# Optimization experiments

Hardware: AMD Instinct MI355X
Metric: run time of the kernel (lower is better)

The kernel has to match this reference:

```python
import math
import jax, jax.numpy as jnp
import numpy as np

TOPK = 2
CAPACITY_FACTOR = 1.25
MIN_CAPACITY = 4


def setup_inputs() -> dict:
    key = jax.random.key(0)
    k1, k2, k3, k4, k5 = jax.random.split(key, 5)
    B, T, H, W, D = 2, 8, 16, 16, 2048
    E, I = 16, 2048
    s = 1.0 / math.sqrt(D)
    return {
        "hidden_states": jax.random.normal(k1, (B, T, H, W, D), dtype=jnp.float32),
        "wg_weight": jax.random.normal(k2, (E, D), dtype=jnp.float32) * s,
        "gate_proj": jax.random.normal(k3, (E, I, D), dtype=jnp.float32) * s,
        "up_proj": jax.random.normal(k4, (E, I, D), dtype=jnp.float32) * s,
        "down_proj": jax.random.normal(k5, (E, D, I), dtype=jnp.float32) * (1.0 / math.sqrt(I)),
    }


def _moe_forward(x, wg, gp, up, dp):
    B, T, H, W, D = x.shape
    S = T * H * W
    # core_shape=(1,1,1): indexing tokens == calculate tokens, flatten (T,H,W)
    tokens = x.reshape(B, S, D).transpose(1, 0, 2).reshape(-1, D)  # (N, D)
    N = tokens.shape[0]
    E = wg.shape[0]

    logits = tokens.astype(jnp.float32) @ wg.T              # (N, E)
    gates = jax.nn.softmax(logits, axis=1)                  # (N, E)

    # static expert capacity: topk * max(ceil(N/E * cf), min_capacity)
    cap = TOPK * max(math.ceil(N / E * CAPACITY_FACTOR), MIN_CAPACITY)

    _, expert_index = jax.lax.top_k(gates, TOPK)            # (N, k)
    expert_mask = jax.nn.one_hot(expert_index, E, dtype=jnp.int32)  # (N, k, E)

    # aux load-balance loss (computed for fidelity)
    mask_aux = expert_mask.max(axis=1).astype(jnp.float32)  # (N, E)
    l_aux = (E ** 2) * jnp.mean(jnp.mean(mask_aux, axis=0) * jnp.mean(gates, axis=0))

    # normalize top-k probabilities (norm_topk_prob=True, topk>1)
    gates_s = jnp.clip(jnp.einsum('nke,ne->n', expert_mask.astype(gates.dtype), gates),
                       jnp.finfo(gates.dtype).eps)
    router_probs = gates / gates_s[:, None]                 # (N, E)

    # token priority: cumsum over (topk*N) flattened in topk-major order
    em = expert_mask.transpose(1, 0, 2).reshape(TOPK * N, E)  # (kN, E)
    tp = jnp.cumsum(em, axis=0) * em - 1
    tp = tp.reshape(TOPK, N, E).transpose(1, 0, 2).max(axis=1)  # (N, E)
    valid = (tp >= 0) & (tp < cap)
    tp = jnp.where(valid, tp, 0)
    dispatch_mask = (tp[:, :, None] == jnp.arange(cap)[None, None, :]) & valid[:, :, None]  # (N,E,C) bool
    combine_weights = router_probs[:, :, None] * dispatch_mask  # (N, E, C)

    # dispatch -> expert FFN (SwiGLU) -> combine
    dm = dispatch_mask.astype(tokens.dtype)
    dispatched = jnp.einsum('nec,nd->ecd', dm, tokens)      # (E, C, D)
    gate_out = jax.nn.silu(jnp.einsum('ecd,eid->eci', dispatched, gp))
    up_out = jnp.einsum('ecd,eid->eci', dispatched, up)
    expert_out = jnp.einsum('eci,edi->ecd', gate_out * up_out, dp)  # (E, C, D)
    combined = jnp.einsum('nec,ecd->nd', combine_weights, expert_out)  # (N, D)

    y = combined.reshape(S, B, D).transpose(1, 0, 2).reshape(B, T, H, W, D)
    return y, l_aux


def reference(hidden_states, wg_weight, gate_proj, up_proj, down_proj):
    y, _l_aux = _moe_forward(hidden_states, wg_weight, gate_proj, up_proj, down_proj)
    return y
```

## Files before the change

### kernel.cpp

```cpp
#include <hip/hip_runtime.h>
#include <hip/hip_bf16.h>
#include <cstdint>
#include <cstddef>

#define NTOK 4096
#define NEXP 16
#define DIM  2048
#define IDIM 2048
#define CAP  640
#define SEQ  2048

typedef float v4f __attribute__((ext_vector_type(4)));
typedef short v8s __attribute__((ext_vector_type(8)));

__device__ __forceinline__ unsigned short f2b(float x) {
    union { float f; unsigned u; } c; c.f = x;
    unsigned r = c.u + 0x7FFFu + ((c.u >> 16) & 1u);
    return (unsigned short)(r >> 16);
}
__device__ __forceinline__ float b2f(unsigned short x) {
    union { unsigned u; float f; } c; c.u = ((unsigned)x) << 16;
    return c.f;
}

__device__ __forceinline__ void async16(const void* g, void* l) {
    __builtin_amdgcn_global_load_lds(
        (const __attribute__((address_space(1))) unsigned int*)g,
        (__attribute__((address_space(3))) unsigned int*)l,
        16, 0, 0);
}

__global__ __launch_bounds__(256) void router_kernel(
    const float* __restrict__ hidden, const float* __restrict__ wg,
    int* __restrict__ top1, int* __restrict__ top2,
    float* __restrict__ w1, float* __restrict__ w2)
{
    int wid  = threadIdx.x >> 6;
    int lane = threadIdx.x & 63;
    int n = blockIdx.x * 4 + wid;
    int e = lane & 15;
    int chunk = lane >> 4;
    const float* tok  = hidden + ((size_t)(n & 1) * SEQ + (n >> 1)) * DIM;
    const float* wrow = wg + (size_t)e * DIM;
    float acc = 0.f;
    int d0 = chunk * (DIM / 4);
    #pragma unroll 4
    for (int d = d0; d < d0 + DIM / 4; d += 4) {
        float4 t4 = *(const float4*)(tok + d);
        float4 g4 = *(const float4*)(wrow + d);
        acc += t4.x * g4.x + t4.y * g4.y + t4.z * g4.z + t4.w * g4.w;
    }
    acc += __shfl_down(acc, 32);
    acc += __shfl_down(acc, 16);
    float v = acc;
    float v1 = v; int i1 = e;
    #pragma unroll
    for (int off = 8; off; off >>= 1) {
        float ov = __shfl_xor(v1, off);
        int   oi = __shfl_xor(i1, off);
        if (ov > v1 || (ov == v1 && oi < i1)) { v1 = ov; i1 = oi; }
    }
    float v2 = (e == i1) ? -INFINITY : v; int i2 = e;
    #pragma unroll
    for (int off = 8; off; off >>= 1) {
        float ov = __shfl_xor(v2, off);
        int   oi = __shfl_xor(i2, off);
        if (ov > v2 || (ov == v2 && oi < i2)) { v2 = ov; i2 = oi; }
    }
    if (lane == 0) {
        float e2v = expf(v2 - v1);
        float inv = 1.f / (1.f + e2v);
        top1[n] = i1; top2[n] = i2;
        w1[n] = inv;  w2[n] = e2v * inv;
    }
}

__global__ __launch_bounds__(1024) void slot_kernel(
    const int* __restrict__ top1, const int* __restrict__ top2,
    int* __restrict__ slot1, int* __restrict__ slot2,
    int* __restrict__ exp_tok, int* __restrict__ counts)
{
    int w = threadIdx.x >> 6;
    int lane = threadIdx.x & 63;
    unsigned long long below = (lane == 0) ? 0ull : ((~0ull) >> (64 - lane));
    int base = 0;
    for (int c = 0; c < NTOK / 64; ++c) {
        int n = c * 64 + lane;
        bool p = (top1[n] == w);
        unsigned long long m = __ballot(p);
        if (p) {
            int s = base + __popcll(m & below);
            slot1[n] = s;
            if (s < CAP) exp_tok[w * CAP + s] = n;
        }
        base += __popcll(m);
    }
    for (int c = 0; c < NTOK / 64; ++c) {
        int n = c * 64 + lane;
        bool p = (top2[n] == w);
        unsigned long long m = __ballot(p);
        if (p) {
            int s = base + __popcll(m & below);
            slot2[n] = s;
            if (s < CAP) exp_tok[w * CAP + s] = n;
        }
        base += __popcll(m);
    }
    if (lane == 0) counts[w] = base < CAP ? base : CAP;
}

__global__ __launch_bounds__(256) void dispatch_kernel(
    const float* __restrict__ hidden, const int* __restrict__ exp_tok,
    const int* __restrict__ counts, unsigned short* __restrict__ disp)
{
    int s = blockIdx.x, e = blockIdx.y;
    unsigned short* dst = disp + ((size_t)e * CAP + s) * DIM + threadIdx.x * 8;
    if (s < counts[e]) {
        int n = exp_tok[e * CAP + s];
        const float* src = hidden + ((size_t)(n & 1) * SEQ + (n >> 1)) * DIM + threadIdx.x * 8;
        float4 a = *(const float4*)src;
        float4 b = *(const float4*)(src + 4);
        v8s o;
        o[0] = (short)f2b(a.x); o[1] = (short)f2b(a.y);
        o[2] = (short)f2b(a.z); o[3] = (short)f2b(a.w);
        o[4] = (short)f2b(b.x); o[5] = (short)f2b(b.y);
        o[6] = (short)f2b(b.z); o[7] = (short)f2b(b.w);
        *(v8s*)dst = o;
    } else {
        v8s z = {0, 0, 0, 0, 0, 0, 0, 0};
        *(v8s*)dst = z;
    }
}

#define BK 64

template<int NW, int ROUNDS>
__device__ __forceinline__ void stage_a(
    const unsigned short* __restrict__ gbase, int grow0, int k0, int rs,
    unsigned short* lds, int wv, int ln)
{
    int sr = ln >> 3;
    int cb = ln & 7;
    #pragma unroll
    for (int p = 0; p < ROUNDS; ++p) {
        int r = p * (NW * 8) + wv * 8 + sr;
        const unsigned short* g = gbase + (size_t)(grow0 + r) * rs + k0 + ((cb ^ (r & 7)) << 3);
        async16(g, lds + (p * (NW * 8) + wv * 8) * 64);
    }
}

template<int NT, int ROUNDS>
__device__ __forceinline__ void issue_bx(
    const float* __restrict__ gbase, int grow0, int k0, int rs,
    float4* regs, int tid)
{
    int cb = tid & 7;
    int r0 = tid >> 3;
    #pragma unroll
    for (int p = 0; p < ROUNDS; ++p) {
        const float* g = gbase + (size_t)(grow0 + p * (NT / 8) + r0) * rs + k0 + (cb << 3);
        regs[2 * p]     = *(const float4*)g;
        regs[2 * p + 1] = *(const float4*)(g + 4);
    }
}

template<int NT, int ROUNDS>
__device__ __forceinline__ void write_bx(
    const float4* regs, unsigned short* lds, int tid)
{
    int cb = tid & 7;
    int r0 = tid >> 3;
    #pragma unroll
    for (int p = 0; p < ROUNDS; ++p) {
        int r = p * (NT / 8) + r0;
        float4 x = regs[2 * p], y = regs[2 * p + 1];
        v8s o;
        o[0] = (short)f2b(x.x); o[1] = (short)f2b(x.y);
        o[2] = (short)f2b(x.z); o[3] = (short)f2b(x.w);
        o[4] = (short)f2b(y.x); o[5] = (short)f2b(y.y);
        o[6] = (short)f2b(y.z); o[7] = (short)f2b(y.w);
        *(v8s*)&lds[r * 64 + ((cb ^ (r & 7)) << 3)] = o;
    }
}

__device__ __forceinline__ void grid_decomp3(int bid, int& mi, int& ni, int& e) {
    int swz = (bid & 7) * 96 + (bid >> 3);
    mi = swz % 3;
    int t = swz / 3;
    ni = t & 15;
    e  = t >> 4;
}

__global__ __launch_bounds__(512, 2) void gateup_kernel(
    const unsigned short* __restrict__ disp, const float* __restrict__ gp,
    const float* __restrict__ up, const int* __restrict__ counts,
    unsigned short* __restrict__ hbuf)
{
    extern __shared__ unsigned short smem[];
    unsigned short* As0 = smem;
    unsigned short* As1 = smem + 16384;
    unsigned short* Bgs = smem + 32768;
    unsigned short* Bus = smem + 40960;
    int mi, ni, e;
    grid_decomp3(blockIdx.x, mi, ni, e);
    int m0 = mi * 256;
    if (m0 >= counts[e]) return;
    int n0 = ni * 128;
    int tid = threadIdx.x;
    int wv = tid >> 6, ln = tid & 63;
    int wm = wv >> 1, wn = wv & 1;
    int lrow = ln & 15, quad = ln >> 4;
    int sw = lrow & 7;

    const unsigned short* Ab = disp + (size_t)e * CAP * DIM;
    const float* Gb = gp + (size_t)e * IDIM * DIM;
    const float* Ub = up + (size_t)e * IDIM * DIM;

    int arow[4], brow[4];
    #pragma unroll
    for (int i = 0; i < 4; ++i) {
        arow[i] = (wm * 64 + i * 16 + lrow) * 64;
        brow[i] = (wn * 64 + i * 16 + lrow) * 64;
    }

    v4f accg[4][4], accu[4][4];
    #pragma unroll
    for (int i = 0; i < 4; ++i)
        #pragma unroll
        for (int j = 0; j < 4; ++j) { accg[i][j] = (v4f)0.f; accu[i][j] = (v4f)0.f; }

    float4 rg[4], ru[4];
    stage_a<8, 4>(Ab, m0, 0, DIM, As0, wv, ln);
    issue_bx<512, 2>(Gb, n0, 0, DIM, rg, tid);
    issue_bx<512, 2>(Ub, n0, 0, DIM, ru, tid);

    for (int k0 = 0; k0 < DIM; k0 += BK) {
        int cur = (k0 >> 6) & 1;
        unsigned short* Ac = cur ? As1 : As0;
        unsigned short* An = cur ? As0 : As1;
        __syncthreads();
        write_bx<512, 2>(rg, Bgs, tid);
        write_bx<512, 2>(ru, Bus, tid);
        __syncthreads();
        int kn = k0 + BK;
        if (kn < DIM) {
            stage_a<8, 4>(Ab, m0, kn, DIM, An, wv, ln);
            issue_bx<512, 2>(Gb, n0, kn, DIM, rg, tid);
            issue_bx<512, 2>(Ub, n0, kn, DIM, ru, tid);
        }
        #pragma unroll
        for (int ks = 0; ks < BK; ks += 32) {
            int cq = ks >> 3;
            v8s a[4];
            #pragma unroll
            for (int i = 0; i < 4; ++i)
                a[i] = *(const v8s*)&Ac[arow[i] + (((cq + quad) ^ sw) << 3)];
            #pragma unroll
            for (int j = 0; j < 4; ++j) {
                v8s bg = *(const v8s*)&Bgs[brow[j] + (((cq + quad) ^ sw) << 3)];
                v8s bu = *(const v8s*)&Bus[brow[j] + (((cq + quad) ^ sw) << 3)];
                #pragma unroll
                for (int i = 0; i < 4; ++i) {
                    accg[i][j] = __builtin_amdgcn_mfma_f32_16x16x32_bf16(a[i], bg, accg[i][j], 0, 0, 0);
                    accu[i][j] = __builtin_amdgcn_mfma_f32_16x16x32_bf16(a[i], bu, accu[i][j], 0, 0, 0);
                }
            }
        }
    }
    unsigned short* hb = hbuf + (size_t)e * CAP * IDIM;
    #pragma unroll
    for (int i = 0; i < 4; ++i)
        #pragma unroll
        for (int j = 0; j < 4; ++j) {
            int row = m0 + wm * 64 + i * 16 + quad * 4;
            int col = n0 + wn * 64 + j * 16 + lrow;
            #pragma unroll
            for (int rg_ = 0; rg_ < 4; ++rg_) {
                if (row + rg_ < CAP) {
                    float g = accg[i][j][rg_], u = accu[i][j][rg_];
                    float hv = (g / (1.f + __expf(-g))) * u;
                    hb[(size_t)(row + rg_) * IDIM + col] = f2b(hv);
                }
            }
        }
}

__global__ __launch_bounds__(256, 2) void down_kernel(
    const unsigned short* __restrict__ hbuf, const float* __restrict__ dp,
    const int* __restrict__ counts, unsigned short* __restrict__ eo)
{
    extern __shared__ unsigned short smem[];
    unsigned short* As0 = smem;
    unsigned short* As1 = smem + 16384;
    unsigned short* Bs  = smem + 32768;
    int mi, ni, e;
    grid_decomp3(blockIdx.x, mi, ni, e);
    int m0 = mi * 256;
    if (m0 >= counts[e]) return;
    int n0 = ni * 128;
    int tid = threadIdx.x;
    int wv = tid >> 6, ln = tid & 63;
    int wm = wv >> 1, wn = wv & 1;
    int lrow = ln & 15, quad = ln >> 4;
    int sw = lrow & 7;

    const unsigned short* Ab = hbuf + (size_t)e * CAP * IDIM;
    const float* Db = dp + (size_t)e * DIM * IDIM;

    int arow[8], brow[4];
    #pragma unroll
    for (int i = 0; i < 8; ++i)
        arow[i] = (wm * 128 + i * 16 + lrow) * 64;
    #pragma unroll
    for (int j = 0; j < 4; ++j)
        brow[j] = (wn * 64 + j * 16 + lrow) * 64;

    v4f acc[8][4];
    #pragma unroll
    for (int i = 0; i < 8; ++i)
        #pragma unroll
        for (int j = 0; j < 4; ++j) acc[i][j] = (v4f)0.f;

    float4 rb[8];
    stage_a<4, 8>(Ab, m0, 0, IDIM, As0, wv, ln);
    issue_bx<256, 4>(Db, n0, 0, IDIM, rb, tid);

    for (int k0 = 0; k0 < IDIM; k0 += BK) {
        int cur = (k0 >> 6) & 1;
        unsigned short* Ac = cur ? As1 : As0;
        unsigned short* An = cur ? As0 : As1;
        __syncthreads();
        write_bx<256, 4>(rb, Bs, tid);
        __syncthreads();
        int kn = k0 + BK;
        if (kn < IDIM) {
            stage_a<4, 8>(Ab, m0, kn, IDIM, An, wv, ln);
            issue_bx<256, 4>(Db, n0, kn, IDIM, rb, tid);
        }
        #pragma unroll
        for (int ks = 0; ks < BK; ks += 32) {
            int cq = ks >> 3;
            v8s a[8];
            #pragma unroll
            for (int i = 0; i < 8; ++i)
                a[i] = *(const v8s*)&Ac[arow[i] + (((cq + quad) ^ sw) << 3)];
            #pragma unroll
            for (int j = 0; j < 4; ++j) {
                v8s b = *(const v8s*)&Bs[brow[j] + (((cq + quad) ^ sw) << 3)];
                #pragma unroll
                for (int i = 0; i < 8; ++i)
                    acc[i][j] = __builtin_amdgcn_mfma_f32_16x16x32_bf16(a[i], b, acc[i][j], 0, 0, 0);
            }
        }
    }
    unsigned short* ob = eo + (size_t)e * CAP * DIM;
    #pragma unroll
    for (int i = 0; i < 8; ++i)
        #pragma unroll
        for (int j = 0; j < 4; ++j) {
            int row = m0 + wm * 128 + i * 16 + quad * 4;
            int col = n0 + wn * 64 + j * 16 + lrow;
            #pragma unroll
            for (int rg_ = 0; rg_ < 4; ++rg_) {
                if (row + rg_ < CAP)
                    ob[(size_t)(row + rg_) * DIM + col] = f2b(acc[i][j][rg_]);
            }
        }
}

__global__ __launch_bounds__(256) void combine_kernel(
    const unsigned short* __restrict__ eo,
    const int* __restrict__ top1, const int* __restrict__ top2,
    const int* __restrict__ slot1, const int* __restrict__ slot2,
    const float* __restrict__ w1, const float* __restrict__ w2,
    float* __restrict__ out)
{
    int n = blockIdx.x;
    int d = threadIdx.x * 8;
    float acc[8];
    #pragma unroll
    for (int i = 0; i < 8; ++i) acc[i] = 0.f;
    int s1 = slot1[n], s2 = slot2[n];
    if (s1 < CAP) {
        const unsigned short* p = eo + ((size_t)top1[n] * CAP + s1) * DIM + d;
        float w = w1[n];
        v8s v = *(const v8s*)p;
        #pragma unroll
        for (int i = 0; i < 8; ++i) acc[i] += w * b2f((unsigned short)v[i]);
    }
    if (s2 < CAP) {
        const unsigned short* p = eo + ((size_t)top2[n] * CAP + s2) * DIM + d;
        float w = w2[n];
        v8s v = *(const v8s*)p;
        #pragma unroll
        for (int i = 0; i < 8; ++i) acc[i] += w * b2f((unsigned short)v[i]);
    }
    float* o = out + ((size_t)(n & 1) * SEQ + (n >> 1)) * DIM + d;
    float4 o0 = {acc[0], acc[1], acc[2], acc[3]};
    float4 o1 = {acc[4], acc[5], acc[6], acc[7]};
    *(float4*)o = o0;
    *(float4*)(o + 4) = o1;
}

extern "C" void kernel_launch(void* const* d_in, const int* in_sizes, int n_in,
                              void* d_out, int out_size, void* d_ws, size_t ws_size,
                              hipStream_t stream) {
    const float* hidden = (const float*)d_in[0];
    const float* wg     = (const float*)d_in[1];
    const float* gp     = (const float*)d_in[2];
    const float* up     = (const float*)d_in[3];
    const float* dp     = (const float*)d_in[4];
    float* out = (float*)d_out;
    char* ws = (char*)d_ws;

    int*   top1    = (int*)(ws + 0);
    int*   top2    = (int*)(ws + 16384);
    float* w1      = (float*)(ws + 32768);
    float* w2      = (float*)(ws + 49152);
    int*   slot1   = (int*)(ws + 65536);
    int*   slot2   = (int*)(ws + 81920);
    int*   counts  = (int*)(ws + 98304);
    int*   exp_tok = (int*)(ws + 98560);
    unsigned short* disp = (unsigned short*)(ws + 262144);
    unsigned short* hbuf = (unsigned short*)(ws + 262144 + 41943040ull);
    unsigned short* eo   = (unsigned short*)(ws + 262144 + 2ull*41943040ull);

    static bool attr_set = false;
    if (!attr_set) {
        hipFuncSetAttribute((const void*)gateup_kernel,
                            hipFuncAttributeMaxDynamicSharedMemorySize, 98304);
        hipFuncSetAttribute((const void*)down_kernel,
                            hipFuncAttributeMaxDynamicSharedMemorySize, 81920);
        attr_set = true;
    }

    const int NB = 3 * 16 * NEXP;

    router_kernel<<<NTOK / 4, 256, 0, stream>>>(hidden, wg, top1, top2, w1, w2);
    slot_kernel<<<1, 1024, 0, stream>>>(top1, top2, slot1, slot2, exp_tok, counts);
    dispatch_kernel<<<dim3(CAP, NEXP), 256, 0, stream>>>(hidden, exp_tok, counts, disp);
    gateup_kernel<<<NB, 512, 98304, stream>>>(disp, gp, up, counts, hbuf);
    down_kernel<<<NB, 256, 81920, stream>>>(hbuf, dp, counts, eo);
    combine_kernel<<<NTOK, 256, 0, stream>>>(eo, top1, top2, slot1, slot2, w1, w2, out);
}
```

Before: 1.048 ms.

## Use packed bf16 convert, single-buffer gate-up A tile, widen down kernel to 512 threads

Replaces the scalar bf16 rounding with the v_cvt_pk_bf16_f32 packed conversion in dispatch and B-tile staging. The gate-up kernel drops A double buffering, staging A synchronously each iteration, which cuts shared memory from 96KB to 64KB to allow more resident blocks. The down kernel moves to 512 threads with 4x4 accumulator tiles per wave, lowering register pressure per thread. Losing the A prefetch in gate-up exposes the global-to-LDS latency each k-step, and the packed convert may round differently from the manual round-to-nearest-even.

```diff
diff --git a/kernel.cpp b/kernel.cpp
--- a/kernel.cpp
+++ b/kernel.cpp
@@ -12,6 +12,7 @@
 
 typedef float v4f __attribute__((ext_vector_type(4)));
 typedef short v8s __attribute__((ext_vector_type(8)));
+typedef unsigned int v4u __attribute__((ext_vector_type(4)));
 
 __device__ __forceinline__ unsigned short f2b(float x) {
     union { float f; unsigned u; } c; c.f = x;
@@ -21,6 +22,11 @@
 __device__ __forceinline__ float b2f(unsigned short x) {
     union { unsigned u; float f; } c; c.u = ((unsigned)x) << 16;
     return c.f;
+}
+__device__ __forceinline__ unsigned cvt2(float a, float b) {
+    unsigned r;
+    asm("v_cvt_pk_bf16_f32 %0, %1, %2" : "=v"(r) : "v"(a), "v"(b));
+    return r;
 }
 
 __device__ __forceinline__ void async16(const void* g, void* l) {
@@ -120,12 +126,10 @@
         const float* src = hidden + ((size_t)(n & 1) * SEQ + (n >> 1)) * DIM + threadIdx.x * 8;
         float4 a = *(const float4*)src;
         float4 b = *(const float4*)(src + 4);
-        v8s o;
-        o[0] = (short)f2b(a.x); o[1] = (short)f2b(a.y);
-        o[2] = (short)f2b(a.z); o[3] = (short)f2b(a.w);
-        o[4] = (short)f2b(b.x); o[5] = (short)f2b(b.y);
-        o[6] = (short)f2b(b.z); o[7] = (short)f2b(b.w);
-        *(v8s*)dst = o;
+        v4u o;
+        o[0] = cvt2(a.x, a.y); o[1] = cvt2(a.z, a.w);
+        o[2] = cvt2(b.x, b.y); o[3] = cvt2(b.z, b.w);
+        *(v4u*)dst = o;
     } else {
         v8s z = {0, 0, 0, 0, 0, 0, 0, 0};
         *(v8s*)dst = z;
@@ -174,12 +178,10 @@
     for (int p = 0; p < ROUNDS; ++p) {
         int r = p * (NT / 8) + r0;
         float4 x = regs[2 * p], y = regs[2 * p + 1];
-        v8s o;
-        o[0] = (short)f2b(x.x); o[1] = (short)f2b(x.y);
-        o[2] = (short)f2b(x.z); o[3] = (short)f2b(x.w);
-        o[4] = (short)f2b(y.x); o[5] = (short)f2b(y.y);
-        o[6] = (short)f2b(y.z); o[7] = (short)f2b(y.w);
-        *(v8s*)&lds[r * 64 + ((cb ^ (r & 7)) << 3)] = o;
+        v4u o;
+        o[0] = cvt2(x.x, x.y); o[1] = cvt2(x.z, x.w);
+        o[2] = cvt2(y.x, y.y); o[3] = cvt2(y.z, y.w);
+        *(v4u*)&lds[r * 64 + ((cb ^ (r & 7)) << 3)] = o;
     }
 }
 
@@ -197,10 +199,9 @@
     unsigned short* __restrict__ hbuf)
 {
     extern __shared__ unsigned short smem[];
-    unsigned short* As0 = smem;
-    unsigned short* As1 = smem + 16384;
-    unsigned short* Bgs = smem + 32768;
-    unsigned short* Bus = smem + 40960;
+    unsigned short* As  = smem;
+    unsigned short* Bgs = smem + 16384;
+    unsigned short* Bus = smem + 24576;
     int mi, ni, e;
     grid_decomp3(blockIdx.x, mi, ni, e);
     int m0 = mi * 256;
@@ -230,21 +231,17 @@
         for (int j = 0; j < 4; ++j) { accg[i][j] = (v4f)0.f; accu[i][j] = (v4f)0.f; }
 
     float4 rg[4], ru[4];
-    stage_a<8, 4>(Ab, m0, 0, DIM, As0, wv, ln);
     issue_bx<512, 2>(Gb, n0, 0, DIM, rg, tid);
     issue_bx<512, 2>(Ub, n0, 0, DIM, ru, tid);
 
     for (int k0 = 0; k0 < DIM; k0 += BK) {
-        int cur = (k0 >> 6) & 1;
-        unsigned short* Ac = cur ? As1 : As0;
-        unsigned short* An = cur ? As0 : As1;
         __syncthreads();
+        stage_a<8, 4>(Ab, m0, k0, DIM, As, wv, ln);
         write_bx<512, 2>(rg, Bgs, tid);
         write_bx<512, 2>(ru, Bus, tid);
         __syncthreads();
         int kn = k0 + BK;
         if (kn < DIM) {
-            stage_a<8, 4>(Ab, m0, kn, DIM, An, wv, ln);
             issue_bx<512, 2>(Gb, n0, kn, DIM, rg, tid);
             issue_bx<512, 2>(Ub, n0, kn, DIM, ru, tid);
         }
@@ -254,7 +251,7 @@
             v8s a[4];
             #pragma unroll
             for (int i = 0; i < 4; ++i)
-                a[i] = *(const v8s*)&Ac[arow[i] + (((cq + quad) ^ sw) << 3)];
+                a[i] = *(const v8s*)&As[arow[i] + (((cq + quad) ^ sw) << 3)];
             #pragma unroll
             for (int j = 0; j < 4; ++j) {
                 v8s bg = *(const v8s*)&Bgs[brow[j] + (((cq + quad) ^ sw) << 3)];
@@ -285,7 +282,7 @@
         }
 }
 
-__global__ __launch_bounds__(256, 2) void down_kernel(
+__global__ __launch_bounds__(512, 2) void down_kernel(
     const unsigned short* __restrict__ hbuf, const float* __restrict__ dp,
     const int* __restrict__ counts, unsigned short* __restrict__ eo)
 {
@@ -307,58 +304,57 @@
     const unsigned short* Ab = hbuf + (size_t)e * CAP * IDIM;
     const float* Db = dp + (size_t)e * DIM * IDIM;
 
-    int arow[8], brow[4];
-    #pragma unroll
-    for (int i = 0; i < 8; ++i)
-        arow[i] = (wm * 128 + i * 16 + lrow) * 64;
-    #pragma unroll
-    for (int j = 0; j < 4; ++j)
-        brow[j] = (wn * 64 + j * 16 + lrow) * 64;
-
-    v4f acc[8][4];
-    #pragma unroll
-    for (int i = 0; i < 8; ++i)
+    int arow[4], brow[4];
+    #pragma unroll
+    for (int i = 0; i < 4; ++i) {
+        arow[i] = (wm * 64 + i * 16 + lrow) * 64;
+        brow[i] = (wn * 64 + i * 16 + lrow) * 64;
+    }
+
+    v4f acc[4][4];
+    #pragma unroll
+    for (int i = 0; i < 4; ++i)
         #pragma unroll
         for (int j = 0; j < 4; ++j) acc[i][j] = (v4f)0.f;
 
-    float4 rb[8];
-    stage_a<4, 8>(Ab, m0, 0, IDIM, As0, wv, ln);
-    issue_bx<256, 4>(Db, n0, 0, IDIM, rb, tid);
+    float4 rb[4];
+    stage_a<8, 4>(Ab, m0, 0, IDIM, As0, wv, ln);
+    issue_bx<512, 2>(Db, n0, 0, IDIM, rb, tid);
 
     for (int k0 = 0; k0 < IDIM; k0 += BK) {
         int cur = (k0 >> 6) & 1;
         unsigned short* Ac = cur ? As1 : As0;
         unsigned short* An = cur ? As0 : As1;
         __syncthreads();
-        write_bx<256, 4>(rb, Bs, tid);
+        write_bx<512, 2>(rb, Bs, tid);
         __syncthreads();
         int kn = k0 + BK;
         if (kn < IDIM) {
-            stage_a<4, 8>(Ab, m0, kn, IDIM, An, wv, ln);
-            issue_bx<256, 4>(Db, n0, kn, IDIM, rb, tid);
+            stage_a<8, 4>(Ab, m0, kn, IDIM, An, wv, ln);
+            issue_bx<512, 2>(Db, n0, kn, IDIM, rb, tid);
         }
         #pragma unroll
         for (int ks = 0; ks < BK; ks += 32) {
             int cq = ks >> 3;
-            v8s a[8];
-            #pragma unroll
-            for (int i = 0; i < 8; ++i)
+            v8s a[4];
+            #pragma unroll
+            for (int i = 0; i < 4; ++i)
                 a[i] = *(const v8s*)&Ac[arow[i] + (((cq + quad) ^ sw) << 3)];
             #pragma unroll
             for (int j = 0; j < 4; ++j) {
                 v8s b = *(const v8s*)&Bs[brow[j] + (((cq + quad) ^ sw) << 3)];
                 #pragma unroll
-                for (int i = 0; i < 8; ++i)
+                for (int i = 0; i < 4; ++i)
                     acc[i][j] = __builtin_amdgcn_mfma_f32_16x16x32_bf16(a[i], b, acc[i][j], 0, 0, 0);
             }
         }
     }
     unsigned short* ob = eo + (size_t)e * CAP * DIM;
     #pragma unroll
-    for (int i = 0; i < 8; ++i)
+    for (int i = 0; i < 4; ++i)
         #pragma unroll
         for (int j = 0; j < 4; ++j) {
-            int row = m0 + wm * 128 + i * 16 + quad * 4;
+            int row = m0 + wm * 64 + i * 16 + quad * 4;
             int col = n0 + wn * 64 + j * 16 + lrow;
             #pragma unroll
             for (int rg_ = 0; rg_ < 4; ++rg_) {
@@ -428,7 +424,7 @@
     static bool attr_set = false;
     if (!attr_set) {
         hipFuncSetAttribute((const void*)gateup_kernel,
-                            hipFuncAttributeMaxDynamicSharedMemorySize, 98304);
+                            hipFuncAttributeMaxDynamicSharedMemorySize, 65536);
         hipFuncSetAttribute((const void*)down_kernel,
                             hipFuncAttributeMaxDynamicSharedMemorySize, 81920);
         attr_set = true;
@@ -439,7 +435,7 @@
     router_kernel<<<NTOK / 4, 256, 0, stream>>>(hidden, wg, top1, top2, w1, w2);
     slot_kernel<<<1, 1024, 0, stream>>>(top1, top2, slot1, slot2, exp_tok, counts);
     dispatch_kernel<<<dim3(CAP, NEXP), 256, 0, stream>>>(hidden, exp_tok, counts, disp);
-    gateup_kernel<<<NB, 512, 98304, stream>>>(disp, gp, up, counts, hbuf);
-    down_kernel<<<NB, 256, 81920, stream>>>(hbuf, dp, counts, eo);
+    gateup_kernel<<<NB, 512, 65536, stream>>>(disp, gp, up, counts, hbuf);
+    down_kernel<<<NB, 512, 81920, stream>>>(hbuf, dp, counts, eo);
     combine_kernel<<<NTOK, 256, 0, stream>>>(eo, top1, top2, slot1, slot2, w1, w2, out);
 }
```

After: 1.074 ms. 1.03x slower.
